# Kernel optimization log

Measured on AMD Instinct MI355X. Metric: run time of the kernel, lower is better.

## Reference

```python
import jax, jax.numpy as jnp
from jax import lax
import numpy as np

HID = 64      # hidden_size
IND = 25      # input_dim = 10 static + 15 dynamic features
HW = 25       # spatial size fixed by fc1 = Linear(12*12*hidden, ...)


def setup_inputs() -> dict:
    key = jax.random.key(0)
    ks = jax.random.split(key, 8)
    def rn(k, shape, s=0.05):
        return jax.random.normal(k, shape, dtype=jnp.float32) * s
    B, T = 64, 24
    return {
        "x": jax.random.normal(ks[0], (B, T, IND, HW, HW), dtype=jnp.float32),
        "ln_g": jnp.ones((IND,), jnp.float32),
        "ln_b": jnp.zeros((IND,), jnp.float32),
        "w_lstm1": rn(ks[1], (4 * HID, IND + HID, 3, 3)),
        "b_lstm1": jnp.zeros((4 * HID,), jnp.float32),
        "w_lstm2": rn(ks[2], (4 * HID, IND + HID, 3, 3)),
        "b_lstm2": jnp.zeros((4 * HID,), jnp.float32),
        "w_conv": rn(ks[3], (HID, 2 * HID, 3, 3)),
        "b_conv": jnp.zeros((HID,), jnp.float32),
        "w_fc1": rn(ks[4], (HID, 12 * 12 * HID)),
        "b_fc1": jnp.zeros((HID,), jnp.float32),
        "w_fc2": rn(ks[5], (HID // 2, HID)),
        "b_fc2": jnp.zeros((HID // 2,), jnp.float32),
        "w_fc3": rn(ks[6], (2, HID // 2)),
        "b_fc3": jnp.zeros((2,), jnp.float32),
    }


def _convlstm(x, w, b, dil):
    # x: (B, T, C, H, W); one ConvLSTM layer, zero-initialized states.
    # Gate order i, f, o, g (standard ndrplz ConvLSTM); same-padding 3x3 conv
    # with rhs dilation `dil` (padding = dil keeps HxW).
    B, _, _, H, W = x.shape
    h0 = jnp.zeros((B, HID, H, W), x.dtype)

    def step(carry, xt):
        h, c = carry
        z = lax.conv_general_dilated(
            jnp.concatenate([xt, h], axis=1), w, (1, 1),
            [(dil, dil), (dil, dil)], rhs_dilation=(dil, dil))
        z = z + b[None, :, None, None]
        i, f, o, g = jnp.split(z, 4, axis=1)
        c = jax.nn.sigmoid(f) * c + jax.nn.sigmoid(i) * jnp.tanh(g)
        h = jax.nn.sigmoid(o) * jnp.tanh(c)
        return (h, c), None

    (h, _), _ = lax.scan(step, (h0, h0), jnp.moveaxis(x, 1, 0))
    return h  # final hidden state (B, HID, H, W)


def reference(x, ln_g, ln_b, w_lstm1, b_lstm1, w_lstm2, b_lstm2,
              w_conv, b_conv, w_fc1, b_fc1, w_fc2, b_fc2, w_fc3, b_fc3):
    # LayerNorm over the channel dim (torch permutes C to last, LN, permutes back)
    mu = jnp.mean(x, axis=2, keepdims=True)
    var = jnp.var(x, axis=2, keepdims=True)
    xn = (x - mu) * lax.rsqrt(var + 1e-5)
    xn = xn * ln_g[None, None, :, None, None] + ln_b[None, None, :, None, None]

    h1 = _convlstm(xn, w_lstm1, b_lstm1, 1)   # dilation 1 branch
    h2 = _convlstm(xn, w_lstm2, b_lstm2, 2)   # dilation 2 branch
    h = jnp.concatenate([h1, h2], axis=1)     # (B, 2*HID, 25, 25)

    h = lax.conv_general_dilated(h, w_conv, (1, 1), [(1, 1), (1, 1)])
    h = jax.nn.relu(h + b_conv[None, :, None, None])
    # max_pool2d(2): floor(25/2)=12 -> VALID window 2 stride 2
    h = lax.reduce_window(h, -jnp.inf, lax.max, (1, 1, 2, 2), (1, 1, 2, 2), 'VALID')
    h = h.reshape(h.shape[0], -1)             # (B, 12*12*HID), channel-major like torch
    h = jax.nn.relu(h @ w_fc1.T + b_fc1)      # dropout is identity at inference
    h = jax.nn.relu(h @ w_fc2.T + b_fc2)
    h = h @ w_fc3.T + b_fc3
    return jax.nn.log_softmax(h, axis=1)
```

## Files before the change

kernel.cpp:

```cpp
#include <hip/hip_runtime.h>
#include <hip/hip_bf16.h>
#include <math.h>

#define B_    64
#define T_    24
#define IND_  25
#define HID_  64
#define NPIX  625

#define WP0   27
#define WP1   29
#define HSTR  72
#define HROWS0 800
#define HROWS1 912
#define HB0   (HROWS0*HSTR)
#define HB1   (HROWS1*HSTR)
#define HB0T  (B_*HB0)
#define HB1T  (B_*HB1)
#define HPART (HB0T+HB1T)

#define WPX   29
#define XROWSU 848
#define XBU   (XROWSU*32)
#define XBUT  (B_*XBU)

#define NRG   9
#define RST0  144
#define RST1  212
#define CH0   (RST0*9)
#define CH1   (RST1*9)

#define HCROWS 832
#define HCB    (HCROWS*128)
#define HCTOT  (B_*HCB)

#define WFRAG_PER_BR (9*3*4*4*512)
#define WFRAG_TOT    (2*WFRAG_PER_BR)

typedef __bf16 bf16x8 __attribute__((ext_vector_type(8)));
typedef float  f32x4  __attribute__((ext_vector_type(4)));
typedef _Float16 f16x4 __attribute__((ext_vector_type(4)));
typedef unsigned short ushort_t;
typedef unsigned int   uint_t;

typedef const __attribute__((address_space(1))) void as1_cvoid;
typedef __attribute__((address_space(3))) void as3_void;

__device__ __forceinline__ float sigmoidf_(float x) { return 1.f / (1.f + __expf(-x)); }
__device__ __forceinline__ float tanh_fast(float x) { return 2.f / (1.f + __expf(-2.f * x)) - 1.f; }
__device__ __forceinline__ ushort_t f2bf(float f) {
    unsigned int u = __float_as_uint(f);
    u += 0x7FFFu + ((u >> 16) & 1u);
    return (ushort_t)(u >> 16);
}

__global__ __launch_bounds__(256) void fill_zero_kernel(uint_t* __restrict__ p, int n) {
    int i = blockIdx.x * 256 + threadIdx.x;
    if (i < n) p[i] = 0u;
}

__global__ __launch_bounds__(256) void repack_w_kernel(
    const float* __restrict__ w1, const float* __restrict__ w2, ushort_t* __restrict__ Wfrag)
{
    int id = blockIdx.x * 256 + threadIdx.x;
    if (id >= WFRAG_TOT) return;
    int e    = id & 7;
    int lane = (id >> 3) & 63;
    int mf   = (id >> 9) & 3;
    int wm   = (id >> 11) & 3;
    int rest = id >> 13;
    int kk   = rest % 3;
    int tap  = (rest / 3) % 9;
    int br   = rest / 27;
    int l16 = lane & 15, kh = lane >> 4;
    int gate = mf;
    int oc   = wm * 16 + l16;
    int k    = kh * 8 + e;
    int c;
    if (kk == 0)      c = (k < IND_) ? k : -1;
    else if (kk == 1) c = IND_ + k;
    else              c = IND_ + 32 + k;
    const float* w = br ? w2 : w1;
    float v = (c >= 0) ? w[((size_t)(gate * 64 + oc) * 89 + c) * 9 + tap] : 0.f;
    Wfrag[id] = f2bf(v);
}

__global__ __launch_bounds__(256) void repack_wc_kernel(
    const float* __restrict__ wc, ushort_t* __restrict__ Wc)
{
    int id = blockIdx.x * 256 + threadIdx.x;
    if (id >= 9 * 64 * 128) return;
    int k   = id % 128;
    int oc  = (id / 128) % 64;
    int tap = id / (128 * 64);
    Wc[id] = f2bf(wc[((size_t)(oc * 128) + k) * 9 + tap]);
}

__global__ __launch_bounds__(256) void ln_t_kernel(
    const float* __restrict__ x, const float* __restrict__ gamma, const float* __restrict__ beta,
    ushort_t* __restrict__ xbu, int t)
{
    int p = blockIdx.x * 256 + threadIdx.x;
    if (p >= B_ * NPIX) return;
    int b = p / NPIX, hw = p % NPIX;
    int y = hw / 25, xx = hw % 25;
    const float* xp = x + ((size_t)(b * T_ + t) * IND_) * NPIX + hw;
    float v[IND_];
    float s = 0.f;
#pragma unroll
    for (int c = 0; c < IND_; ++c) { v[c] = xp[c * NPIX]; s += v[c]; }
    float mu = s * (1.f / IND_);
    float ss = 0.f;
#pragma unroll
    for (int c = 0; c < IND_; ++c) { float d = v[c] - mu; ss += d * d; }
    float rstd = rsqrtf(ss * (1.f / IND_) + 1e-5f);
    ushort_t* o = xbu + (size_t)b * XBU + (size_t)((y + 2) * WPX + (xx + 2)) * 32;
#pragma unroll
    for (int c = 0; c < IND_; ++c)
        o[c] = f2bf((v[c] - mu) * rstd * gamma[c] + beta[c]);
}

__global__ __launch_bounds__(512, 4) void convlstm_mfma_kernel(
    const float* __restrict__ x, const float* __restrict__ ln_g, const float* __restrict__ ln_b,
    ushort_t* __restrict__ xbu,
    const ushort_t* __restrict__ h0c, const ushort_t* __restrict__ h1c,
    ushort_t* __restrict__ h0n, ushort_t* __restrict__ h1n,
    const ushort_t* __restrict__ Wfrag,
    const float* __restrict__ bias1, const float* __restrict__ bias2,
    ushort_t* __restrict__ cst, int t)
{
    const int rg = blockIdx.x;
    const int b  = blockIdx.y;
    const int br = blockIdx.z;
    const int d  = 1 + br;
    const int Wp = 25 + 2 * d;
    const int par = t & 1, nxt = par ^ 1;
    const ushort_t* __restrict__ hc = (br ? h1c + (size_t)b * HB1 : h0c + (size_t)b * HB0);
    ushort_t* __restrict__ hn       = (br ? h1n + (size_t)b * HB1 : h0n + (size_t)b * HB0);
    const ushort_t* __restrict__ xg = xbu + (size_t)par * XBUT + (size_t)b * XBU;
    const float* __restrict__ bias = br ? bias2 : bias1;
    const ushort_t* __restrict__ WFb = Wfrag + (size_t)br * WFRAG_PER_BR;
    f16x4* __restrict__ cb4 = (f16x4*)cst + (size_t)(br * B_ + b) * 16 * NPIX;

    __shared__ ushort_t tile[RST1 * HSTR];

    const int tid = threadIdx.x;
    const int u0  = rg * 3 * Wp;
    const int CH  = br ? CH1 : CH0;
    const int wave_u = tid & 448;

    {
        const char* gsrc = (const char*)(hc + (size_t)u0 * HSTR);
#pragma unroll
        for (int j = 0; j < 4; ++j) {
            const int i = j * 512 + tid;
            if (i < CH) {
                __builtin_amdgcn_global_load_lds(
                    (as1_cvoid*)(gsrc + (size_t)i * 16),
                    (as3_void*)((char*)tile + (size_t)(j * 512 + wave_u) * 16),
                    16, 0, 0);
            }
        }
    }
    if (t + 1 < T_ && tid < 35) {
        const int linbid = (br * B_ + b) * NRG + rg;
        const int p = linbid * 35 + tid;
        if (p < B_ * NPIX) {
            const int bb = p / NPIX, hw = p - bb * NPIX;
            const int y = hw / 25, xx = hw - y * 25;
            const float* xp = x + ((size_t)(bb * T_ + t + 1) * IND_) * NPIX + hw;
            float v[IND_];
            float s = 0.f;
#pragma unroll
            for (int c = 0; c < IND_; ++c) { v[c] = xp[c * NPIX]; s += v[c]; }
            const float mu = s * (1.f / IND_);
            float ss = 0.f;
#pragma unroll
            for (int c = 0; c < IND_; ++c) { float dd = v[c] - mu; ss += dd * dd; }
            const float rstd = rsqrtf(ss * (1.f / IND_) + 1e-5f);
            ushort_t us[IND_];
#pragma unroll
            for (int c = 0; c < IND_; ++c) us[c] = f2bf((v[c] - mu) * rstd * ln_g[c] + ln_b[c]);
            uint4 q0, q1, q2;
            q0.x = us[0] | ((uint_t)us[1] << 16);   q0.y = us[2] | ((uint_t)us[3] << 16);
            q0.z = us[4] | ((uint_t)us[5] << 16);   q0.w = us[6] | ((uint_t)us[7] << 16);
            q1.x = us[8] | ((uint_t)us[9] << 16);   q1.y = us[10] | ((uint_t)us[11] << 16);
            q1.z = us[12] | ((uint_t)us[13] << 16); q1.w = us[14] | ((uint_t)us[15] << 16);
            q2.x = us[16] | ((uint_t)us[17] << 16); q2.y = us[18] | ((uint_t)us[19] << 16);
            q2.z = us[20] | ((uint_t)us[21] << 16); q2.w = us[22] | ((uint_t)us[23] << 16);
            ushort_t* o = xbu + (size_t)nxt * XBUT + (size_t)bb * XBU
                          + (size_t)((y + 2) * WPX + (xx + 2)) * 32;
            *(uint4*)o = q0; *(uint4*)(o + 8) = q1; *(uint4*)(o + 16) = q2; o[24] = us[24];
        }
    }
    __syncthreads();

    const int w    = tid >> 6, lane = tid & 63;
    const int wm   = w & 3, wn = w >> 2;
    const int l16  = lane & 15, kh = lane >> 4;
    const int koff = kh * 8;

    f32x4 acc[4][3];
#pragma unroll
    for (int i = 0; i < 4; ++i)
#pragma unroll
        for (int j = 0; j < 3; ++j) acc[i][j] = (f32x4){0.f, 0.f, 0.f, 0.f};

    int baserel[3];
    int basex[3];
#pragma unroll
    for (int nf = 0; nf < 3; ++nf) {
        int n = wn * 48 + nf * 16 + l16;
        const int rit = n >> 5, xxa = n & 31;
        baserel[nf] = rit * Wp + xxa;
        basex[nf] = ((rg * 3 + rit + 2) * WPX + (xxa + 2)) * 32 + koff;
    }

    const ushort_t* __restrict__ WTb = WFb + wm * 2048 + lane * 8;
    bf16x8 af[2][4];
#pragma unroll
    for (int mf = 0; mf < 4; ++mf)
        af[0][mf] = *(const bf16x8*)(WTb + mf * 512);

#pragma unroll
    for (int u = 0; u < 27; ++u) {
        if (u + 1 < 27) {
#pragma unroll
            for (int mf = 0; mf < 4; ++mf)
                af[(u + 1) & 1][mf] =
                    *(const bf16x8*)(WTb + (size_t)(u + 1) * 8192 + mf * 512);
        }
        const int tap = u / 3, kk = u - 3 * (u / 3);
        const int ky = tap / 3, kx = tap - 3 * ky;
        bf16x8 bfr[3];
        if (kk == 0) {
            const int toffx = ((ky - 1) * WPX + (kx - 1)) * d * 32;
#pragma unroll
            for (int nf = 0; nf < 3; ++nf)
                bfr[nf] = *(const bf16x8*)(xg + (size_t)(basex[nf] + toffx));
        } else {
            const int toff = (ky * Wp + kx) * d;
#pragma unroll
            for (int nf = 0; nf < 3; ++nf)
                bfr[nf] = *(const bf16x8*)(tile + (baserel[nf] + toff) * HSTR
                                           + (kk - 1) * 32 + koff);
        }
#pragma unroll
        for (int mf = 0; mf < 4; ++mf)
#pragma unroll
            for (int nf = 0; nf < 3; ++nf)
                acc[mf][nf] = __builtin_amdgcn_mfma_f32_16x16x32_bf16(
                    af[u & 1][mf], bfr[nf], acc[mf][nf], 0, 0, 0);
    }

    const int oc0 = wm * 16 + kh * 4;
    const int ocq = wm * 4 + kh;
    float bi4[4], bf4[4], bo4[4], bg4[4];
#pragma unroll
    for (int r = 0; r < 4; ++r) {
        bi4[r] = bias[oc0 + r];
        bf4[r] = bias[64 + oc0 + r];
        bo4[r] = bias[128 + oc0 + r];
        bg4[r] = bias[192 + oc0 + r];
    }
#pragma unroll
    for (int nf = 0; nf < 3; ++nf) {
        const int n = wn * 48 + nf * 16 + l16;
        const int xx = n & 31;
        if (xx >= 25) continue;
        const int y = rg * 3 + (n >> 5);
        if (y >= 25) continue;
        const int pix = y * 25 + xx;
        f16x4* cp = cb4 + (size_t)ocq * NPIX + pix;
        f16x4 cvh;
        if (t != 0) cvh = *cp;
        else        cvh = (f16x4){0, 0, 0, 0};
        ushort_t hs[4];
#pragma unroll
        for (int r = 0; r < 4; ++r) {
            const float zi = acc[0][nf][r] + bi4[r];
            const float zf = acc[1][nf][r] + bf4[r];
            const float zo = acc[2][nf][r] + bo4[r];
            const float zg = acc[3][nf][r] + bg4[r];
            const float cn = sigmoidf_(zf) * (float)cvh[r] + sigmoidf_(zi) * tanh_fast(zg);
            cvh[r] = (_Float16)cn;
            hs[r] = f2bf(sigmoidf_(zo) * tanh_fast(cn));
        }
        *cp = cvh;
        uint2 hv;
        hv.x = (uint_t)hs[0] | ((uint_t)hs[1] << 16);
        hv.y = (uint_t)hs[2] | ((uint_t)hs[3] << 16);
        *(uint2*)(hn + (size_t)((y + d) * Wp + (xx + d)) * HSTR + oc0) = hv;
    }
}

__global__ __launch_bounds__(256) void combine_h_kernel(
    const ushort_t* __restrict__ h0, const ushort_t* __restrict__ h1, ushort_t* __restrict__ Hc)
{
    int id = blockIdx.x * 256 + threadIdx.x;
    if (id >= B_ * NPIX * 128) return;
    int k   = id % 128;
    int pix = (id / 128) % NPIX;
    int b   = id / (128 * NPIX);
    int y = pix / 25, xx = pix % 25;
    ushort_t v;
    if (k < 64) v = h0[(size_t)b * HB0 + (size_t)((y + 1) * WP0 + (xx + 1)) * HSTR + k];
    else        v = h1[(size_t)b * HB1 + (size_t)((y + 2) * WP1 + (xx + 2)) * HSTR + (k - 64)];
    Hc[(size_t)b * HCB + (size_t)((y + 1) * 27 + (xx + 1)) * 128 + k] = v;
}

__global__ __launch_bounds__(512) void conv_mfma_kernel(
    const ushort_t* __restrict__ Hc, const ushort_t* __restrict__ Wc,
    const float* __restrict__ bc, float* __restrict__ conv_out)
{
    const int rg = blockIdx.x;
    const int b  = blockIdx.y;
    const ushort_t* __restrict__ Hb = Hc + (size_t)b * HCB;

    const int tid  = threadIdx.x;
    const int w    = tid >> 6, lane = tid & 63;
    const int wm   = w & 1, wn = w >> 1;
    const int l16  = lane & 15, kh = lane >> 4;
    const int koff = kh * 8;

    f32x4 acc[2][2];
#pragma unroll
    for (int i = 0; i < 2; ++i)
#pragma unroll
        for (int j = 0; j < 2; ++j) acc[i][j] = (f32x4){0.f, 0.f, 0.f, 0.f};

    int baserow[2];
#pragma unroll
    for (int nf = 0; nf < 2; ++nf) {
        int n = wn * 32 + nf * 16 + l16;
        baserow[nf] = (rg * 4 + (n >> 5)) * 27 + (n & 31);
    }
    const ushort_t* __restrict__ Wm = Wc + (size_t)(wm * 32 + l16) * 128 + koff;

    for (int tap = 0; tap < 9; ++tap) {
        const int ky = tap / 3, kx = tap - 3 * ky;
        const int toff = ky * 27 + kx;
        const ushort_t* __restrict__ Wt = Wm + (size_t)tap * (64 * 128);
        const ushort_t* Urow[2];
#pragma unroll
        for (int nf = 0; nf < 2; ++nf)
            Urow[nf] = Hb + (size_t)(baserow[nf] + toff) * 128 + koff;
#pragma unroll
        for (int kk = 0; kk < 4; ++kk) {
            bf16x8 af[2], bfr[2];
#pragma unroll
            for (int mf = 0; mf < 2; ++mf)
                af[mf] = *(const bf16x8*)(Wt + mf * 16 * 128 + kk * 32);
#pragma unroll
            for (int nf = 0; nf < 2; ++nf)
                bfr[nf] = *(const bf16x8*)(Urow[nf] + kk * 32);
#pragma unroll
            for (int mf = 0; mf < 2; ++mf)
#pragma unroll
                for (int nf = 0; nf < 2; ++nf)
                    acc[mf][nf] = __builtin_amdgcn_mfma_f32_16x16x32_bf16(
                        af[mf], bfr[nf], acc[mf][nf], 0, 0, 0);
        }
    }

#pragma unroll
    for (int mf = 0; mf < 2; ++mf) {
#pragma unroll
        for (int nf = 0; nf < 2; ++nf) {
            const int n = wn * 32 + nf * 16 + l16;
            const int xx = n & 31;
            if (xx >= 25) continue;
            const int y = rg * 4 + wn;
            if (y >= 25) continue;
#pragma unroll
            for (int r = 0; r < 4; ++r) {
                const int oc = wm * 32 + mf * 16 + kh * 4 + r;
                const float v = fmaxf(acc[mf][nf][r] + bc[oc], 0.f);
                conv_out[((size_t)(b * 64 + oc)) * NPIX + y * 25 + xx] = v;
            }
        }
    }
}

__global__ __launch_bounds__(256) void pool_kernel(
    const float* __restrict__ conv_out, float* __restrict__ pool)
{
    int id = blockIdx.x * 256 + threadIdx.x;
    if (id >= B_ * 64 * 144) return;
    int px = id % 12;
    int py = (id / 12) % 12;
    int oc = (id / 144) % 64;
    int b  = id / (144 * 64);
    const float* p = conv_out + ((size_t)(b * 64 + oc)) * NPIX;
    const int cy = 2 * py, cx = 2 * px;
    float mx = fmaxf(fmaxf(p[cy * 25 + cx], p[cy * 25 + cx + 1]),
                     fmaxf(p[(cy + 1) * 25 + cx], p[(cy + 1) * 25 + cx + 1]));
    pool[(size_t)b * 9216 + oc * 144 + py * 12 + px] = mx;
}

__global__ __launch_bounds__(256) void fc1_kernel(
    const float* __restrict__ pool, const float* __restrict__ w1, const float* __restrict__ b1,
    float* __restrict__ f1)
{
    const int task = blockIdx.x * 4 + (threadIdx.x >> 6);
    const int lane = threadIdx.x & 63;
    const int b = task >> 6, oc = task & 63;
    const float* pr = pool + (size_t)b * 9216;
    const float* wr = w1 + (size_t)oc * 9216;
    float acc = 0.f;
#pragma unroll 4
    for (int it = 0; it < 36; ++it) {
        const int k = it * 256 + lane * 4;
        const float4 p = *(const float4*)(pr + k);
        const float4 ww = *(const float4*)(wr + k);
        acc += p.x * ww.x + p.y * ww.y + p.z * ww.z + p.w * ww.w;
    }
#pragma unroll
    for (int off = 32; off > 0; off >>= 1) acc += __shfl_down(acc, off);
    if (lane == 0) f1[b * 64 + oc] = fmaxf(acc + b1[oc], 0.f);
}

__global__ __launch_bounds__(64) void head2_kernel(
    const float* __restrict__ f1,
    const float* __restrict__ w2, const float* __restrict__ b2,
    const float* __restrict__ w3, const float* __restrict__ b3,
    float* __restrict__ out)
{
    const int b = blockIdx.x;
    __shared__ float f1l[64];
    __shared__ float f2[32];
    const int tid = threadIdx.x;
    f1l[tid] = f1[b * 64 + tid];
    __syncthreads();
    if (tid < 32) {
        float acc = b2[tid];
        const float* wr = w2 + (size_t)tid * 64;
#pragma unroll
        for (int k = 0; k < 64; ++k) acc += f1l[k] * wr[k];
        f2[tid] = fmaxf(acc, 0.f);
    }
    __syncthreads();
    if (tid == 0) {
        float y0 = b3[0], y1 = b3[1];
#pragma unroll
        for (int k = 0; k < 32; ++k) { y0 += f2[k] * w3[k]; y1 += f2[k] * w3[32 + k]; }
        const float m = fmaxf(y0, y1);
        const float lse = m + logf(expf(y0 - m) + expf(y1 - m));
        out[b * 2 + 0] = y0 - lse;
        out[b * 2 + 1] = y1 - lse;
    }
}

extern "C" void kernel_launch(void* const* d_in, const int* in_sizes, int n_in,
                              void* d_out, int out_size, void* d_ws, size_t ws_size,
                              hipStream_t stream) {
    const float* x    = (const float*)d_in[0];
    const float* ln_g = (const float*)d_in[1];
    const float* ln_b = (const float*)d_in[2];
    const float* w_l1 = (const float*)d_in[3];
    const float* b_l1 = (const float*)d_in[4];
    const float* w_l2 = (const float*)d_in[5];
    const float* b_l2 = (const float*)d_in[6];
    const float* w_c  = (const float*)d_in[7];
    const float* b_c  = (const float*)d_in[8];
    const float* w_f1 = (const float*)d_in[9];
    const float* b_f1 = (const float*)d_in[10];
    const float* w_f2 = (const float*)d_in[11];
    const float* b_f2 = (const float*)d_in[12];
    const float* w_f3 = (const float*)d_in[13];
    const float* b_f3 = (const float*)d_in[14];

    ushort_t* wsu = (ushort_t*)d_ws;
    uint_t*   wsi = (uint_t*)d_ws;

    ushort_t* xbu = wsu;
    ushort_t* h0A = xbu + 2 * (size_t)XBUT;
    ushort_t* h1A = h0A + HB0T;
    ushort_t* h0B = h1A + HB1T;
    ushort_t* h1B = h0B + HB0T;
    ushort_t* cst = h1B + HB1T;
    ushort_t* Wfrag = cst + 5120000;
    ushort_t* Wc    = Wfrag + WFRAG_TOT;
    float*    f1    = (float*)(Wc + 73728);
    ushort_t* Hc    = h0B;
    float*    conv_out = (float*)cst;
    float*    pool  = (float*)wsu;

    const size_t zt = 2 * (size_t)XBUT + 2 * (size_t)HPART;
    fill_zero_kernel<<<((int)(zt / 2) + 255) / 256, 256, 0, stream>>>(wsi, (int)(zt / 2));
    repack_w_kernel<<<(WFRAG_TOT + 255) / 256, 256, 0, stream>>>(w_l1, w_l2, Wfrag);
    repack_wc_kernel<<<(9 * 64 * 128 + 255) / 256, 256, 0, stream>>>(w_c, Wc);

    ln_t_kernel<<<(B_ * NPIX + 255) / 256, 256, 0, stream>>>(x, ln_g, ln_b, xbu, 0);

    ushort_t* H0[2] = {h0A, h0B};
    ushort_t* H1[2] = {h1A, h1B};
    for (int t = 0; t < T_; ++t) {
        const int cur = t & 1, nxt = cur ^ 1;
        convlstm_mfma_kernel<<<dim3(NRG, B_, 2), 512, 0, stream>>>(
            x, ln_g, ln_b, xbu,
            H0[cur], H1[cur], H0[nxt], H1[nxt], Wfrag, b_l1, b_l2, cst, t);
    }
    fill_zero_kernel<<<(HCTOT / 2 + 255) / 256, 256, 0, stream>>>((uint_t*)Hc, HCTOT / 2);
    combine_h_kernel<<<(B_ * NPIX * 128 + 255) / 256, 256, 0, stream>>>(h0A, h1A, Hc);
    conv_mfma_kernel<<<dim3(7, B_), 512, 0, stream>>>(Hc, Wc, b_c, conv_out);
    pool_kernel<<<(B_ * 64 * 144 + 255) / 256, 256, 0, stream>>>(conv_out, pool);
    fc1_kernel<<<1024, 256, 0, stream>>>(pool, w_f1, b_f1, f1);
    head2_kernel<<<B_, 64, 0, stream>>>(f1, w_f2, b_f2, w_f3, b_f3, (float*)d_out);
}
```

Baseline: 2.087 ms.

## Stage input tile in LDS and cut row groups with a wider final group

Each block now copies its slice of the normalized input (nine padded rows) into shared memory with async global-to-LDS loads, so the input taps read from LDS instead of global memory. The grid drops from nine to eight row groups, and the last group handles four output rows through a templated body with four N-fragments. The per-block prefetch of next-step LayerNorm pixels grows to 40 to keep full coverage. The weight-fragment double buffering is removed. In exchange, shared memory per block grows substantially, which may lower occupancy, and the last row group does more work than the others, which unbalances the load.

```diff
diff --git a/kernel.cpp b/kernel.cpp
--- a/kernel.cpp
+++ b/kernel.cpp
@@ -20,15 +20,14 @@
 #define HPART (HB0T+HB1T)
 
 #define WPX   29
-#define XROWSU 848
+#define XRW   928
+#define XROWSU 880
 #define XBU   (XROWSU*32)
 #define XBUT  (B_*XBU)
 
-#define NRG   9
-#define RST0  144
-#define RST1  212
-#define CH0   (RST0*9)
-#define CH1   (RST1*9)
+#define NRG   8
+#define RSTMAX 240
+#define XTROWS 9
 
 #define HCROWS 832
 #define HCB    (HCROWS*128)
@@ -120,6 +119,105 @@
         o[c] = f2bf((v[c] - mu) * rstd * gamma[c] + beta[c]);
 }
 
+template<int NF>
+__device__ __forceinline__ void conv_body(
+    int rg, int d, int Wp, int t, int tid,
+    const ushort_t* __restrict__ xt, const ushort_t* __restrict__ tile,
+    ushort_t* __restrict__ hn, const ushort_t* __restrict__ WFb,
+    const float* __restrict__ bias, f16x4* __restrict__ cb4)
+{
+    const int w    = tid >> 6, lane = tid & 63;
+    const int wm   = w & 3, wn = w >> 2;
+    const int l16  = lane & 15, kh = lane >> 4;
+    const int koff = kh * 8;
+
+    f32x4 acc[4][NF];
+#pragma unroll
+    for (int i = 0; i < 4; ++i)
+#pragma unroll
+        for (int j = 0; j < NF; ++j) acc[i][j] = (f32x4){0.f, 0.f, 0.f, 0.f};
+
+    int baserel[NF];
+    int basexl[NF];
+#pragma unroll
+    for (int nf = 0; nf < NF; ++nf) {
+        int n = wn * (NF * 16) + nf * 16 + l16;
+        const int rit = n >> 5, xxa = n & 31;
+        baserel[nf] = rit * Wp + xxa;
+        basexl[nf]  = (rit + 2) * XRW + (xxa + 2) * 32 + koff;
+    }
+
+    const ushort_t* __restrict__ WTb = WFb + wm * 2048 + lane * 8;
+
+#pragma unroll
+    for (int u = 0; u < 27; ++u) {
+        const int tap = u / 3, kk = u - 3 * (u / 3);
+        const int ky = tap / 3, kx = tap - 3 * ky;
+        bf16x8 af[4], bfr[NF];
+#pragma unroll
+        for (int mf = 0; mf < 4; ++mf)
+            af[mf] = *(const bf16x8*)(WTb + (size_t)u * 8192 + mf * 512);
+        if (kk == 0) {
+            const int toffx = ((ky - 1) * WPX + (kx - 1)) * d * 32;
+#pragma unroll
+            for (int nf = 0; nf < NF; ++nf)
+                bfr[nf] = *(const bf16x8*)(xt + (size_t)(basexl[nf] + toffx));
+        } else {
+            const int toff = (ky * Wp + kx) * d;
+#pragma unroll
+            for (int nf = 0; nf < NF; ++nf)
+                bfr[nf] = *(const bf16x8*)(tile + (baserel[nf] + toff) * HSTR
+                                           + (kk - 1) * 32 + koff);
+        }
+#pragma unroll
+        for (int mf = 0; mf < 4; ++mf)
+#pragma unroll
+            for (int nf = 0; nf < NF; ++nf)
+                acc[mf][nf] = __builtin_amdgcn_mfma_f32_16x16x32_bf16(
+                    af[mf], bfr[nf], acc[mf][nf], 0, 0, 0);
+    }
+
+    const int oc0 = wm * 16 + kh * 4;
+    const int ocq = wm * 4 + kh;
+    float bi4[4], bf4[4], bo4[4], bg4[4];
+#pragma unroll
+    for (int r = 0; r < 4; ++r) {
+        bi4[r] = bias[oc0 + r];
+        bf4[r] = bias[64 + oc0 + r];
+        bo4[r] = bias[128 + oc0 + r];
+        bg4[r] = bias[192 + oc0 + r];
+    }
+#pragma unroll
+    for (int nf = 0; nf < NF; ++nf) {
+        const int n = wn * (NF * 16) + nf * 16 + l16;
+        const int xx = n & 31;
+        if (xx >= 25) continue;
+        const int y = rg * 3 + (n >> 5);
+        if (y >= 25) continue;
+        const int pix = y * 25 + xx;
+        f16x4* cp = cb4 + (size_t)ocq * NPIX + pix;
+        f16x4 cvh;
+        if (t != 0) cvh = *cp;
+        else        cvh = (f16x4){0, 0, 0, 0};
+        ushort_t hs[4];
+#pragma unroll
+        for (int r = 0; r < 4; ++r) {
+            const float zi = acc[0][nf][r] + bi4[r];
+            const float zf = acc[1][nf][r] + bf4[r];
+            const float zo = acc[2][nf][r] + bo4[r];
+            const float zg = acc[3][nf][r] + bg4[r];
+            const float cn = sigmoidf_(zf) * (float)cvh[r] + sigmoidf_(zi) * tanh_fast(zg);
+            cvh[r] = (_Float16)cn;
+            hs[r] = f2bf(sigmoidf_(zo) * tanh_fast(cn));
+        }
+        *cp = cvh;
+        uint2 hv;
+        hv.x = (uint_t)hs[0] | ((uint_t)hs[1] << 16);
+        hv.y = (uint_t)hs[2] | ((uint_t)hs[3] << 16);
+        *(uint2*)(hn + (size_t)((y + d) * Wp + (xx + d)) * HSTR + oc0) = hv;
+    }
+}
+
 __global__ __launch_bounds__(512, 4) void convlstm_mfma_kernel(
     const float* __restrict__ x, const float* __restrict__ ln_g, const float* __restrict__ ln_b,
     ushort_t* __restrict__ xbu,
@@ -137,22 +235,23 @@
     const int par = t & 1, nxt = par ^ 1;
     const ushort_t* __restrict__ hc = (br ? h1c + (size_t)b * HB1 : h0c + (size_t)b * HB0);
     ushort_t* __restrict__ hn       = (br ? h1n + (size_t)b * HB1 : h0n + (size_t)b * HB0);
-    const ushort_t* __restrict__ xg = xbu + (size_t)par * XBUT + (size_t)b * XBU;
     const float* __restrict__ bias = br ? bias2 : bias1;
     const ushort_t* __restrict__ WFb = Wfrag + (size_t)br * WFRAG_PER_BR;
     f16x4* __restrict__ cb4 = (f16x4*)cst + (size_t)(br * B_ + b) * 16 * NPIX;
 
-    __shared__ ushort_t tile[RST1 * HSTR];
+    __shared__ ushort_t tile[RSTMAX * HSTR];
+    __shared__ ushort_t xt[XTROWS * XRW];
 
     const int tid = threadIdx.x;
     const int u0  = rg * 3 * Wp;
-    const int CH  = br ? CH1 : CH0;
+    const int NF4 = (rg == NRG - 1);
+    const int CH  = NF4 ? (br ? 2160 : 1548) : (br ? 1908 : 1296);
     const int wave_u = tid & 448;
 
     {
         const char* gsrc = (const char*)(hc + (size_t)u0 * HSTR);
 #pragma unroll
-        for (int j = 0; j < 4; ++j) {
+        for (int j = 0; j < 5; ++j) {
             const int i = j * 512 + tid;
             if (i < CH) {
                 __builtin_amdgcn_global_load_lds(
@@ -162,9 +261,23 @@
             }
         }
     }
-    if (t + 1 < T_ && tid < 35) {
+    {
+        const char* gsrc = (const char*)(xbu + (size_t)par * XBUT + (size_t)b * XBU
+                                         + (size_t)(rg * 3) * XRW);
+#pragma unroll
+        for (int j = 0; j < 3; ++j) {
+            const int i = j * 512 + tid;
+            if (i < (XTROWS * XRW) / 8) {
+                __builtin_amdgcn_global_load_lds(
+                    (as1_cvoid*)(gsrc + (size_t)i * 16),
+                    (as3_void*)((char*)xt + (size_t)(j * 512 + wave_u) * 16),
+                    16, 0, 0);
+            }
+        }
+    }
+    if (t + 1 < T_ && tid < 40) {
         const int linbid = (br * B_ + b) * NRG + rg;
-        const int p = linbid * 35 + tid;
+        const int p = linbid * 40 + tid;
         if (p < B_ * NPIX) {
             const int bb = p / NPIX, hw = p - bb * NPIX;
             const int y = hw / 25, xx = hw - y * 25;
@@ -195,103 +308,10 @@
     }
     __syncthreads();
 
-    const int w    = tid >> 6, lane = tid & 63;
-    const int wm   = w & 3, wn = w >> 2;
-    const int l16  = lane & 15, kh = lane >> 4;
-    const int koff = kh * 8;
-
-    f32x4 acc[4][3];
-#pragma unroll
-    for (int i = 0; i < 4; ++i)
-#pragma unroll
-        for (int j = 0; j < 3; ++j) acc[i][j] = (f32x4){0.f, 0.f, 0.f, 0.f};
-
-    int baserel[3];
-    int basex[3];
-#pragma unroll
-    for (int nf = 0; nf < 3; ++nf) {
-        int n = wn * 48 + nf * 16 + l16;
-        const int rit = n >> 5, xxa = n & 31;
-        baserel[nf] = rit * Wp + xxa;
-        basex[nf] = ((rg * 3 + rit + 2) * WPX + (xxa + 2)) * 32 + koff;
-    }
-
-    const ushort_t* __restrict__ WTb = WFb + wm * 2048 + lane * 8;
-    bf16x8 af[2][4];
-#pragma unroll
-    for (int mf = 0; mf < 4; ++mf)
-        af[0][mf] = *(const bf16x8*)(WTb + mf * 512);
-
-#pragma unroll
-    for (int u = 0; u < 27; ++u) {
-        if (u + 1 < 27) {
-#pragma unroll
-            for (int mf = 0; mf < 4; ++mf)
-                af[(u + 1) & 1][mf] =
-                    *(const bf16x8*)(WTb + (size_t)(u + 1) * 8192 + mf * 512);
-        }
-        const int tap = u / 3, kk = u - 3 * (u / 3);
-        const int ky = tap / 3, kx = tap - 3 * ky;
-        bf16x8 bfr[3];
-        if (kk == 0) {
-            const int toffx = ((ky - 1) * WPX + (kx - 1)) * d * 32;
-#pragma unroll
-            for (int nf = 0; nf < 3; ++nf)
-                bfr[nf] = *(const bf16x8*)(xg + (size_t)(basex[nf] + toffx));
-        } else {
-            const int toff = (ky * Wp + kx) * d;
-#pragma unroll
-            for (int nf = 0; nf < 3; ++nf)
-                bfr[nf] = *(const bf16x8*)(tile + (baserel[nf] + toff) * HSTR
-                                           + (kk - 1) * 32 + koff);
-        }
-#pragma unroll
-        for (int mf = 0; mf < 4; ++mf)
-#pragma unroll
-            for (int nf = 0; nf < 3; ++nf)
-                acc[mf][nf] = __builtin_amdgcn_mfma_f32_16x16x32_bf16(
-                    af[u & 1][mf], bfr[nf], acc[mf][nf], 0, 0, 0);
-    }
-
-    const int oc0 = wm * 16 + kh * 4;
-    const int ocq = wm * 4 + kh;
-    float bi4[4], bf4[4], bo4[4], bg4[4];
-#pragma unroll
-    for (int r = 0; r < 4; ++r) {
-        bi4[r] = bias[oc0 + r];
-        bf4[r] = bias[64 + oc0 + r];
-        bo4[r] = bias[128 + oc0 + r];
-        bg4[r] = bias[192 + oc0 + r];
-    }
-#pragma unroll
-    for (int nf = 0; nf < 3; ++nf) {
-        const int n = wn * 48 + nf * 16 + l16;
-        const int xx = n & 31;
-        if (xx >= 25) continue;
-        const int y = rg * 3 + (n >> 5);
-        if (y >= 25) continue;
-        const int pix = y * 25 + xx;
-        f16x4* cp = cb4 + (size_t)ocq * NPIX + pix;
-        f16x4 cvh;
-        if (t != 0) cvh = *cp;
-        else        cvh = (f16x4){0, 0, 0, 0};
-        ushort_t hs[4];
-#pragma unroll
-        for (int r = 0; r < 4; ++r) {
-            const float zi = acc[0][nf][r] + bi4[r];
-            const float zf = acc[1][nf][r] + bf4[r];
-            const float zo = acc[2][nf][r] + bo4[r];
-            const float zg = acc[3][nf][r] + bg4[r];
-            const float cn = sigmoidf_(zf) * (float)cvh[r] + sigmoidf_(zi) * tanh_fast(zg);
-            cvh[r] = (_Float16)cn;
-            hs[r] = f2bf(sigmoidf_(zo) * tanh_fast(cn));
-        }
-        *cp = cvh;
-        uint2 hv;
-        hv.x = (uint_t)hs[0] | ((uint_t)hs[1] << 16);
-        hv.y = (uint_t)hs[2] | ((uint_t)hs[3] << 16);
-        *(uint2*)(hn + (size_t)((y + d) * Wp + (xx + d)) * HSTR + oc0) = hv;
-    }
+    if (NF4)
+        conv_body<4>(rg, d, Wp, t, tid, xt, tile, hn, WFb, bias, cb4);
+    else
+        conv_body<3>(rg, d, Wp, t, tid, xt, tile, hn, WFb, bias, cb4);
 }
 
 __global__ __launch_bounds__(256) void combine_h_kernel(
```

Result: slower. 2.244 ms (+7.5%).
